# Kernel optimization log

Hardware: AMD Instinct MI355X
Metric: run time of the kernel (lower is better)

The kernel has to match this reference:

```python
import jax, jax.numpy as jnp
import numpy as np
from jax import lax

M, N, Q = 256, 65536, 64
LAMBDA_STAR = 0.1
LAMBDA_O = 0.1
T_ITERS = 16
PM_ITERS = 100


def setup_inputs() -> dict:
    key = jax.random.key(0)
    kx, kd = jax.random.split(key)
    X = jax.random.normal(kx, (M, N), dtype=jnp.float32)
    D = jax.random.normal(kd, (M, Q), dtype=jnp.float32)
    return {"X": X, "D": D}


def _power_method(D):
    # Largest eigenvalue of D^T D via 100-step power iteration (fixed random init).
    x0 = jax.random.normal(jax.random.key(1), (1, Q), dtype=D.dtype)

    def step(x, _):
        x = (x @ D.T) @ D          # [1,q] -> [1,m] -> [1,q]
        nm = jnp.linalg.norm(x)
        return x / nm, nm

    _, nms = lax.scan(step, x0, None, length=PM_ITERS)
    return nms[-1]


def reference(X, D):
    m, n = X.shape
    q = D.shape[1]
    alpha = _power_method(D)
    eta = 1.0 / alpha

    Iq = jnp.eye(q, dtype=D.dtype)
    Im = jnp.eye(m, dtype=D.dtype)
    top = jnp.concatenate([D.T @ D + LAMBDA_STAR * Iq, D.T], axis=1)   # [q, q+m]
    bot = jnp.concatenate([D, (1.0 + LAMBDA_STAR) * Im], axis=1)       # [m, q+m]
    H = jnp.eye(m + q, dtype=D.dtype) - eta * jnp.concatenate([top, bot], axis=0)
    W = eta * jnp.concatenate([D.T, Im], axis=0)                        # [(m+q), m]
    t = LAMBDA_O * eta * jnp.concatenate([jnp.zeros(q, D.dtype), jnp.ones(m, D.dtype)])

    b0 = W @ X                                                           # [(m+q), n]
    Z0 = jnp.zeros((m + q, n), dtype=X.dtype)

    def ista_step(carry, _):
        Z, b = carry
        Znew = jnp.maximum(0.0, b - t[:, None])    # thresholding (ger(t, ones) == t broadcast)
        b = b + H @ (Znew - Z)
        return (Znew, b), None

    (Z, _), _ = lax.scan(ista_step, (Z0, b0), None, length=T_ITERS)
    return Z
```

## Files before the change

kernel.cpp:

```cpp
#include <hip/hip_runtime.h>


typedef __bf16 bf16x8 __attribute__((ext_vector_type(8)));
typedef float f32x4 __attribute__((ext_vector_type(4)));

#define MFMA16(a, b, c) __builtin_amdgcn_mfma_f32_16x16x32_bf16((a), (b), (c), 0, 0, 0)

#define NTOT 65536
#define NCOL 32

__device__ __forceinline__ unsigned pk2(float a, float b) {
  unsigned short ua = __builtin_bit_cast(unsigned short, (__bf16)a);
  unsigned short ub = __builtin_bit_cast(unsigned short, (__bf16)b);
  return (unsigned)ua | ((unsigned)ub << 16);
}

__global__ void rnmf_prep(const float* __restrict__ D, void* __restrict__ ws) {
  float* wsf = (float*)ws;
  __bf16* Dbf = (__bf16*)((char*)ws + 256);
  __bf16* DTbf = (__bf16*)((char*)ws + 256 + 32768);

  __shared__ __bf16 DTl[64 * 264];
  __shared__ __bf16 gA[64 * 72];
  __shared__ __bf16 gB[64 * 72];
  __shared__ float gf[64 * 68];
  __shared__ __align__(16) float xv[64];

  const int tid = threadIdx.x;
  const int w = tid >> 6, lane = tid & 63, c = lane & 15, q4 = lane >> 4;

#pragma unroll
  for (int e = 0; e < 16; ++e) {
    int i4 = e * 256 + tid;
    float4 dv = *(const float4*)(D + i4 * 4);
    uint2 u; u.x = pk2(dv.x, dv.y); u.y = pk2(dv.z, dv.w);
    *(uint2*)(Dbf + i4 * 4) = u;
  }
#pragma unroll
  for (int e = 0; e < 64; ++e) {
    int flat = e * 256 + tid;
    int k = flat >> 6, a = flat & 63;
    DTl[a * 264 + k] = (__bf16)D[k * 64 + a];
  }
  __syncthreads();
#pragma unroll
  for (int e = 0; e < 8; ++e) {
    int fi = e * 256 + tid;
    int a = fi >> 5;
    int k = (fi * 8) & 255;
    *(bf16x8*)(DTbf + fi * 8) = *(const bf16x8*)&DTl[a * 264 + k];
  }
#pragma unroll
  for (int ct = 0; ct < 4; ++ct) {
    f32x4 acc = {0.f, 0.f, 0.f, 0.f};
#pragma unroll
    for (int kb = 0; kb < 8; ++kb) {
      bf16x8 a = *(const bf16x8*)&DTl[(16 * w + c) * 264 + 32 * kb + 8 * q4];
      bf16x8 b = *(const bf16x8*)&DTl[(16 * ct + c) * 264 + 32 * kb + 8 * q4];
      acc = MFMA16(a, b, acc);
    }
#pragma unroll
    for (int r = 0; r < 4; ++r)
      gA[(16 * w + 4 * q4 + r) * 72 + 16 * ct + c] = (__bf16)acc[r];
  }
  __syncthreads();
#pragma unroll
  for (int ct = 0; ct < 4; ++ct) {
    f32x4 acc = {0.f, 0.f, 0.f, 0.f};
#pragma unroll
    for (int kb = 0; kb < 2; ++kb) {
      bf16x8 a = *(const bf16x8*)&gA[(16 * w + c) * 72 + 32 * kb + 8 * q4];
      bf16x8 b = *(const bf16x8*)&gA[(16 * ct + c) * 72 + 32 * kb + 8 * q4];
      acc = MFMA16(a, b, acc);
    }
#pragma unroll
    for (int r = 0; r < 4; ++r)
      gB[(16 * w + 4 * q4 + r) * 72 + 16 * ct + c] = (__bf16)acc[r];
  }
  __syncthreads();
#pragma unroll
  for (int ct = 0; ct < 4; ++ct) {
    f32x4 acc = {0.f, 0.f, 0.f, 0.f};
#pragma unroll
    for (int kb = 0; kb < 2; ++kb) {
      bf16x8 a = *(const bf16x8*)&gB[(16 * w + c) * 72 + 32 * kb + 8 * q4];
      bf16x8 b = *(const bf16x8*)&gB[(16 * ct + c) * 72 + 32 * kb + 8 * q4];
      acc = MFMA16(a, b, acc);
    }
#pragma unroll
    for (int r = 0; r < 4; ++r)
      gA[(16 * w + 4 * q4 + r) * 72 + 16 * ct + c] = (__bf16)acc[r];
  }
  __syncthreads();
#pragma unroll
  for (int ct = 0; ct < 4; ++ct) {
    f32x4 acc = {0.f, 0.f, 0.f, 0.f};
#pragma unroll
    for (int kb = 0; kb < 2; ++kb) {
      bf16x8 a = *(const bf16x8*)&gA[(16 * w + c) * 72 + 32 * kb + 8 * q4];
      bf16x8 b = *(const bf16x8*)&gA[(16 * ct + c) * 72 + 32 * kb + 8 * q4];
      acc = MFMA16(a, b, acc);
    }
#pragma unroll
    for (int r = 0; r < 4; ++r)
      gf[(16 * w + 4 * q4 + r) * 68 + 16 * ct + c] = acc[r];
  }
  __syncthreads();

  if (w == 0) {
    float td = gf[lane * 68 + lane];
#pragma unroll
    for (int off = 32; off; off >>= 1) td += __shfl_xor(td, off, 64);
    const float tr = td;
    const float itr = 1.f / tr;
    xv[lane] = 1.f;
    float nm = 1.f;
    for (int itp = 0; itp < 28; ++itp) {
      float acc = 0.f;
#pragma unroll
      for (int k = 0; k < 64; k += 4) {
        float4 g = *(const float4*)&gf[lane * 68 + k];
        float4 xx = *(const float4*)&xv[k];
        acc = fmaf(g.x, xx.x, acc);
        acc = fmaf(g.y, xx.y, acc);
        acc = fmaf(g.z, xx.z, acc);
        acc = fmaf(g.w, xx.w, acc);
      }
      float y = acc * itr;
      float n2 = y * y;
#pragma unroll
      for (int off = 32; off; off >>= 1) n2 += __shfl_xor(n2, off, 64);
      nm = sqrtf(n2);
      xv[lane] = y / nm;
    }
    if (lane == 0) wsf[0] = 1.f / powf(nm * tr, 0.125f);
  }
}

__global__ __launch_bounds__(256, 2) void rnmf_main(const float* __restrict__ X,
                                                    float* __restrict__ Z,
                                                    const void* __restrict__ ws) {
  const float* wsf = (const float*)ws;
  const __bf16* Dbf = (const __bf16*)((const char*)ws + 256);
  const __bf16* DTbf = (const __bf16*)((const char*)ws + 256 + 32768);

  __shared__ __bf16 zqb[32 * 72];
  __shared__ __bf16 vb[32 * 264];
  __shared__ float xs[32 * 260];

  const int tid = threadIdx.x;
  const int w = tid >> 6;
  const int lane = tid & 63;
  const int c = lane & 15;
  const int q4 = lane >> 4;
  const int j0 = blockIdx.x * NCOL;

#pragma unroll
  for (int e = 0; e < 32; ++e) {
    int flat = e * 256 + tid;
    int row = flat >> 5, col = flat & 31;
    xs[col * 260 + row] = X[row * NTOT + j0 + col];
  }

  const float eta = wsf[0];
  const float cq = 1.f - 0.1f * eta;
  const float cm = 1.f - 1.1f * eta;
  const float tm = 0.1f * eta;

  bf16x8 d1[4][2];
#pragma unroll
  for (int rt = 0; rt < 4; ++rt)
#pragma unroll
    for (int kb = 0; kb < 2; ++kb)
      d1[rt][kb] = *(const bf16x8*)(Dbf + (64 * w + 16 * rt + c) * 64 + 32 * kb + 8 * q4);
  bf16x8 d2[8];
#pragma unroll
  for (int kb = 0; kb < 8; ++kb)
    d2[kb] = *(const bf16x8*)(DTbf + (16 * w + c) * 256 + 32 * kb + 8 * q4);

  __syncthreads();

  float bqt[2][4];
#pragma unroll
  for (int ct = 0; ct < 2; ++ct) {
    f32x4 acc = {0.f, 0.f, 0.f, 0.f};
#pragma unroll
    for (int kb = 0; kb < 8; ++kb) {
      const float* p = &xs[(16 * ct + c) * 260 + 32 * kb + 8 * q4];
      float4 lo = *(const float4*)p;
      float4 hi = *(const float4*)(p + 4);
      bf16x8 bf;
      bf[0] = (__bf16)lo.x; bf[1] = (__bf16)lo.y; bf[2] = (__bf16)lo.z; bf[3] = (__bf16)lo.w;
      bf[4] = (__bf16)hi.x; bf[5] = (__bf16)hi.y; bf[6] = (__bf16)hi.z; bf[7] = (__bf16)hi.w;
      acc = MFMA16(d2[kb], bf, acc);
    }
#pragma unroll
    for (int r = 0; r < 4; ++r) bqt[ct][r] = eta * acc[r];
  }

  float bmt[4][2][4];
#pragma unroll
  for (int rt = 0; rt < 4; ++rt)
#pragma unroll
    for (int ct = 0; ct < 2; ++ct) {
      const float* p = &xs[(16 * ct + c) * 260 + 64 * w + 16 * rt + 4 * q4];
      float4 v = *(const float4*)p;
      bmt[rt][ct][0] = fmaf(eta, v.x, -tm);
      bmt[rt][ct][1] = fmaf(eta, v.y, -tm);
      bmt[rt][ct][2] = fmaf(eta, v.z, -tm);
      bmt[rt][ct][3] = fmaf(eta, v.w, -tm);
    }

  float zq[2][4], zm[4][2][4];
#pragma unroll
  for (int ct = 0; ct < 2; ++ct)
#pragma unroll
    for (int r = 0; r < 4; ++r) zq[ct][r] = fmaxf(bqt[ct][r], 0.f);
#pragma unroll
  for (int rt = 0; rt < 4; ++rt)
#pragma unroll
    for (int ct = 0; ct < 2; ++ct)
#pragma unroll
      for (int r = 0; r < 4; ++r) zm[rt][ct][r] = fmaxf(bmt[rt][ct][r], 0.f);

#pragma unroll
  for (int ct = 0; ct < 2; ++ct) {
    uint2 u; u.x = pk2(zq[ct][0], zq[ct][1]); u.y = pk2(zq[ct][2], zq[ct][3]);
    *(uint2*)&zqb[(16 * ct + c) * 72 + 16 * w + 4 * q4] = u;
  }

  for (int it = 0; it < 15; ++it) {
    __syncthreads();
#pragma unroll
    for (int ct = 0; ct < 2; ++ct) {
      bf16x8 bz0 = *(const bf16x8*)&zqb[(16 * ct + c) * 72 + 8 * q4];
      bf16x8 bz1 = *(const bf16x8*)&zqb[(16 * ct + c) * 72 + 32 + 8 * q4];
#pragma unroll
      for (int rt = 0; rt < 4; ++rt) {
        f32x4 acc = {0.f, 0.f, 0.f, 0.f};
        acc = MFMA16(d1[rt][0], bz0, acc);
        acc = MFMA16(d1[rt][1], bz1, acc);
        float vv[4];
#pragma unroll
        for (int r = 0; r < 4; ++r) {
          float u = acc[r];
          float zo = zm[rt][ct][r];
          vv[r] = u + zo;
          float zn = fmaf(cm, zo, bmt[rt][ct][r]);
          zn = fmaf(-eta, u, zn);
          zm[rt][ct][r] = fmaxf(zn, 0.f);
        }
        uint2 uu; uu.x = pk2(vv[0], vv[1]); uu.y = pk2(vv[2], vv[3]);
        *(uint2*)&vb[(16 * ct + c) * 264 + 64 * w + 16 * rt + 4 * q4] = uu;
      }
    }
    __syncthreads();
#pragma unroll
    for (int ct = 0; ct < 2; ++ct) {
      f32x4 acc = {0.f, 0.f, 0.f, 0.f};
#pragma unroll
      for (int kb = 0; kb < 8; ++kb) {
        bf16x8 bv = *(const bf16x8*)&vb[(16 * ct + c) * 264 + 32 * kb + 8 * q4];
        acc = MFMA16(d2[kb], bv, acc);
      }
#pragma unroll
      for (int r = 0; r < 4; ++r) {
        float zn = fmaf(cq, zq[ct][r], bqt[ct][r]);
        zn = fmaf(-eta, acc[r], zn);
        zq[ct][r] = fmaxf(zn, 0.f);
      }
      uint2 u; u.x = pk2(zq[ct][0], zq[ct][1]); u.y = pk2(zq[ct][2], zq[ct][3]);
      *(uint2*)&zqb[(16 * ct + c) * 72 + 16 * w + 4 * q4] = u;
    }
  }

#pragma unroll
  for (int ct = 0; ct < 2; ++ct)
#pragma unroll
    for (int r = 0; r < 4; ++r)
      Z[(16 * w + 4 * q4 + r) * NTOT + j0 + 16 * ct + c] = zq[ct][r];
#pragma unroll
  for (int rt = 0; rt < 4; ++rt)
#pragma unroll
    for (int ct = 0; ct < 2; ++ct)
#pragma unroll
      for (int r = 0; r < 4; ++r)
        Z[(64 + 64 * w + 16 * rt + 4 * q4 + r) * NTOT + j0 + 16 * ct + c] = zm[rt][ct][r];
}

extern "C" void kernel_launch(void* const* d_in, const int* in_sizes, int n_in,
                              void* d_out, int out_size, void* d_ws, size_t ws_size,
                              hipStream_t stream) {
  const float* X = (const float*)d_in[0];
  const float* D = (const float*)d_in[1];
  float* Z = (float*)d_out;
  rnmf_prep<<<dim3(1), dim3(256), 0, stream>>>(D, d_ws);
  rnmf_main<<<dim3(NTOT / NCOL), dim3(256), 0, stream>>>(X, Z, d_ws);
}
```

Before: 243.4 us.

## Pack f32 math, reuse shared arena, fragment-order LDS layout, raise occupancy

The main kernel now puts all its shared buffers in one arena and reuses the X staging space for the z/v bf16 operands. Those operands are stored in MFMA fragment order, so each lane reads its 16 bytes contiguously. The elementwise ISTA update now uses packed two-wide f32 FMA/max with hardware bf16 pack conversion, X is loaded as float4, and launch bounds go from 2 to 3 blocks per CU. The prep kernel pads the Gram matrix rows to avoid LDS bank conflicts. Smaller LDS use and packed ALU ops aim at higher occupancy and fewer VALU instructions, at the cost of register pressure under the tighter bound.

```diff
diff --git a/kernel.cpp b/kernel.cpp
--- a/kernel.cpp
+++ b/kernel.cpp
@@ -2,7 +2,9 @@
 
 
 typedef __bf16 bf16x8 __attribute__((ext_vector_type(8)));
+typedef __bf16 bf16x2 __attribute__((ext_vector_type(2)));
 typedef float f32x4 __attribute__((ext_vector_type(4)));
+typedef float f32x2 __attribute__((ext_vector_type(2)));
 
 #define MFMA16(a, b, c) __builtin_amdgcn_mfma_f32_16x16x32_bf16((a), (b), (c), 0, 0, 0)
 
@@ -10,11 +12,24 @@
 #define NCOL 32
 
 __device__ __forceinline__ unsigned pk2(float a, float b) {
+#if __has_builtin(__builtin_amdgcn_cvt_pk_bf16_f32)
+  return __builtin_bit_cast(unsigned, __builtin_amdgcn_cvt_pk_bf16_f32(a, b));
+#else
   unsigned short ua = __builtin_bit_cast(unsigned short, (__bf16)a);
   unsigned short ub = __builtin_bit_cast(unsigned short, (__bf16)b);
   return (unsigned)ua | ((unsigned)ub << 16);
-}
-
+#endif
+}
+__device__ __forceinline__ unsigned pk2v(f32x2 v) { return pk2(v[0], v[1]); }
+__device__ __forceinline__ f32x2 f2(float s) { f32x2 v = {s, s}; return v; }
+__device__ __forceinline__ f32x2 pfma(f32x2 a, f32x2 b, f32x2 c) {
+  return __builtin_elementwise_fma(a, b, c);
+}
+__device__ __forceinline__ f32x2 pmax0(f32x2 a) {
+  return __builtin_elementwise_max(a, f2(0.f));
+}
+
+#define GOF(row) ((row) * 68 + (((row) >> 3) << 2))
 __global__ void rnmf_prep(const float* __restrict__ D, void* __restrict__ ws) {
   float* wsf = (float*)ws;
   __bf16* Dbf = (__bf16*)((char*)ws + 256);
@@ -23,7 +38,7 @@
   __shared__ __bf16 DTl[64 * 264];
   __shared__ __bf16 gA[64 * 72];
   __shared__ __bf16 gB[64 * 72];
-  __shared__ float gf[64 * 68];
+  __shared__ float gf[64 * 68 + 32];
   __shared__ __align__(16) float xv[64];
 
   const int tid = threadIdx.x;
@@ -103,23 +118,24 @@
     }
 #pragma unroll
     for (int r = 0; r < 4; ++r)
-      gf[(16 * w + 4 * q4 + r) * 68 + 16 * ct + c] = acc[r];
+      gf[GOF(16 * w + 4 * q4 + r) + 16 * ct + c] = acc[r];
   }
   __syncthreads();
 
   if (w == 0) {
-    float td = gf[lane * 68 + lane];
+    float td = gf[GOF(lane) + lane];
 #pragma unroll
     for (int off = 32; off; off >>= 1) td += __shfl_xor(td, off, 64);
     const float tr = td;
     const float itr = 1.f / tr;
     xv[lane] = 1.f;
     float nm = 1.f;
+    const int rowoff = GOF(lane);
     for (int itp = 0; itp < 28; ++itp) {
       float acc = 0.f;
 #pragma unroll
       for (int k = 0; k < 64; k += 4) {
-        float4 g = *(const float4*)&gf[lane * 68 + k];
+        float4 g = *(const float4*)&gf[rowoff + k];
         float4 xx = *(const float4*)&xv[k];
         acc = fmaf(g.x, xx.x, acc);
         acc = fmaf(g.y, xx.y, acc);
@@ -137,34 +153,40 @@
   }
 }
 
-__global__ __launch_bounds__(256, 2) void rnmf_main(const float* __restrict__ X,
+__global__ __launch_bounds__(256, 3) void rnmf_main(const float* __restrict__ X,
                                                     float* __restrict__ Z,
                                                     const void* __restrict__ ws) {
   const float* wsf = (const float*)ws;
   const __bf16* Dbf = (const __bf16*)((const char*)ws + 256);
   const __bf16* DTbf = (const __bf16*)((const char*)ws + 256 + 32768);
 
-  __shared__ __bf16 zqb[32 * 72];
-  __shared__ __bf16 vb[32 * 264];
-  __shared__ float xs[32 * 260];
+  __shared__ __align__(16) char arena[33280];
+  float* xs = (float*)arena;
 
   const int tid = threadIdx.x;
   const int w = tid >> 6;
   const int lane = tid & 63;
   const int c = lane & 15;
   const int q4 = lane >> 4;
+  const int q4h = q4 >> 1, q4l = q4 & 1;
   const int j0 = blockIdx.x * NCOL;
 
 #pragma unroll
-  for (int e = 0; e < 32; ++e) {
-    int flat = e * 256 + tid;
-    int row = flat >> 5, col = flat & 31;
-    xs[col * 260 + row] = X[row * NTOT + j0 + col];
+  for (int e = 0; e < 8; ++e) {
+    int idx = e * 256 + tid;
+    int row = idx >> 3, c4 = (idx & 7) * 4;
+    float4 g = *(const float4*)(X + row * NTOT + j0 + c4);
+    xs[(c4 + 0) * 260 + row] = g.x;
+    xs[(c4 + 1) * 260 + row] = g.y;
+    xs[(c4 + 2) * 260 + row] = g.z;
+    xs[(c4 + 3) * 260 + row] = g.w;
   }
 
   const float eta = wsf[0];
-  const float cq = 1.f - 0.1f * eta;
-  const float cm = 1.f - 1.1f * eta;
+  const f32x2 etav = f2(eta);
+  const f32x2 metav = f2(-eta);
+  const f32x2 cqv = f2(1.f - 0.1f * eta);
+  const f32x2 cmv = f2(1.f - 1.1f * eta);
   const float tm = 0.1f * eta;
 
   bf16x8 d1[4][2];
@@ -180,7 +202,7 @@
 
   __syncthreads();
 
-  float bqt[2][4];
+  f32x2 bqt2[2][2];
 #pragma unroll
   for (int ct = 0; ct < 2; ++ct) {
     f32x4 acc = {0.f, 0.f, 0.f, 0.f};
@@ -189,69 +211,73 @@
       const float* p = &xs[(16 * ct + c) * 260 + 32 * kb + 8 * q4];
       float4 lo = *(const float4*)p;
       float4 hi = *(const float4*)(p + 4);
-      bf16x8 bf;
-      bf[0] = (__bf16)lo.x; bf[1] = (__bf16)lo.y; bf[2] = (__bf16)lo.z; bf[3] = (__bf16)lo.w;
-      bf[4] = (__bf16)hi.x; bf[5] = (__bf16)hi.y; bf[6] = (__bf16)hi.z; bf[7] = (__bf16)hi.w;
-      acc = MFMA16(d2[kb], bf, acc);
-    }
-#pragma unroll
-    for (int r = 0; r < 4; ++r) bqt[ct][r] = eta * acc[r];
-  }
-
-  float bmt[4][2][4];
+      unsigned p0 = pk2(lo.x, lo.y), p1 = pk2(lo.z, lo.w);
+      unsigned p2 = pk2(hi.x, hi.y), p3 = pk2(hi.z, hi.w);
+      uint4 packed = {p0, p1, p2, p3};
+      acc = MFMA16(d2[kb], __builtin_bit_cast(bf16x8, packed), acc);
+    }
+    f32x2 a0 = {acc[0], acc[1]}, a1 = {acc[2], acc[3]};
+    bqt2[ct][0] = etav * a0;
+    bqt2[ct][1] = etav * a1;
+  }
+
+  f32x2 bmt2[4][2][2];
 #pragma unroll
   for (int rt = 0; rt < 4; ++rt)
 #pragma unroll
     for (int ct = 0; ct < 2; ++ct) {
       const float* p = &xs[(16 * ct + c) * 260 + 64 * w + 16 * rt + 4 * q4];
       float4 v = *(const float4*)p;
-      bmt[rt][ct][0] = fmaf(eta, v.x, -tm);
-      bmt[rt][ct][1] = fmaf(eta, v.y, -tm);
-      bmt[rt][ct][2] = fmaf(eta, v.z, -tm);
-      bmt[rt][ct][3] = fmaf(eta, v.w, -tm);
-    }
-
-  float zq[2][4], zm[4][2][4];
+      f32x2 x0 = {v.x, v.y}, x1 = {v.z, v.w};
+      bmt2[rt][ct][0] = pfma(etav, x0, f2(-tm));
+      bmt2[rt][ct][1] = pfma(etav, x1, f2(-tm));
+    }
+
+  __syncthreads();
+
+  f32x2 zq2[2][2], zm2[4][2][2];
 #pragma unroll
   for (int ct = 0; ct < 2; ++ct)
 #pragma unroll
-    for (int r = 0; r < 4; ++r) zq[ct][r] = fmaxf(bqt[ct][r], 0.f);
+    for (int p = 0; p < 2; ++p) zq2[ct][p] = pmax0(bqt2[ct][p]);
 #pragma unroll
   for (int rt = 0; rt < 4; ++rt)
 #pragma unroll
     for (int ct = 0; ct < 2; ++ct)
 #pragma unroll
-      for (int r = 0; r < 4; ++r) zm[rt][ct][r] = fmaxf(bmt[rt][ct][r], 0.f);
+      for (int p = 0; p < 2; ++p) zm2[rt][ct][p] = pmax0(bmt2[rt][ct][p]);
+
+  char* smem = arena;
+  const int rb = lane * 16;
+  const int wzq = (w >> 1) * 1024 + ((2 * w) & 3) * 256 + q4h * 256 + c * 16 + 8 * q4l;
+  const int wvb = 4096 + 2 * w * 1024 + q4h * 256 + c * 16 + 8 * q4l;
 
 #pragma unroll
   for (int ct = 0; ct < 2; ++ct) {
-    uint2 u; u.x = pk2(zq[ct][0], zq[ct][1]); u.y = pk2(zq[ct][2], zq[ct][3]);
-    *(uint2*)&zqb[(16 * ct + c) * 72 + 16 * w + 4 * q4] = u;
+    uint2 u; u.x = pk2v(zq2[ct][0]); u.y = pk2v(zq2[ct][1]);
+    *(uint2*)(smem + wzq + ct * 2048) = u;
   }
 
   for (int it = 0; it < 15; ++it) {
     __syncthreads();
 #pragma unroll
     for (int ct = 0; ct < 2; ++ct) {
-      bf16x8 bz0 = *(const bf16x8*)&zqb[(16 * ct + c) * 72 + 8 * q4];
-      bf16x8 bz1 = *(const bf16x8*)&zqb[(16 * ct + c) * 72 + 32 + 8 * q4];
+      bf16x8 bz0 = *(const bf16x8*)(smem + rb + ct * 2048);
+      bf16x8 bz1 = *(const bf16x8*)(smem + rb + ct * 2048 + 1024);
 #pragma unroll
       for (int rt = 0; rt < 4; ++rt) {
         f32x4 acc = {0.f, 0.f, 0.f, 0.f};
         acc = MFMA16(d1[rt][0], bz0, acc);
         acc = MFMA16(d1[rt][1], bz1, acc);
-        float vv[4];
-#pragma unroll
-        for (int r = 0; r < 4; ++r) {
-          float u = acc[r];
-          float zo = zm[rt][ct][r];
-          vv[r] = u + zo;
-          float zn = fmaf(cm, zo, bmt[rt][ct][r]);
-          zn = fmaf(-eta, u, zn);
-          zm[rt][ct][r] = fmaxf(zn, 0.f);
-        }
-        uint2 uu; uu.x = pk2(vv[0], vv[1]); uu.y = pk2(vv[2], vv[3]);
-        *(uint2*)&vb[(16 * ct + c) * 264 + 64 * w + 16 * rt + 4 * q4] = uu;
+        f32x2 u0 = {acc[0], acc[1]}, u1 = {acc[2], acc[3]};
+        f32x2 z0 = zm2[rt][ct][0], z1 = zm2[rt][ct][1];
+        f32x2 v0 = u0 + z0, v1 = u1 + z1;
+        f32x2 t0 = pfma(cmv, z0, bmt2[rt][ct][0]);
+        f32x2 t1 = pfma(cmv, z1, bmt2[rt][ct][1]);
+        zm2[rt][ct][0] = pmax0(pfma(metav, u0, t0));
+        zm2[rt][ct][1] = pmax0(pfma(metav, u1, t1));
+        uint2 uu; uu.x = pk2v(v0); uu.y = pk2v(v1);
+        *(uint2*)(smem + wvb + ct * 8192 + rt * 512) = uu;
       }
     }
     __syncthreads();
@@ -260,32 +286,35 @@
       f32x4 acc = {0.f, 0.f, 0.f, 0.f};
 #pragma unroll
       for (int kb = 0; kb < 8; ++kb) {
-        bf16x8 bv = *(const bf16x8*)&vb[(16 * ct + c) * 264 + 32 * kb + 8 * q4];
+        bf16x8 bv = *(const bf16x8*)(smem + rb + 4096 + ct * 8192 + kb * 1024);
         acc = MFMA16(d2[kb], bv, acc);
       }
-#pragma unroll
-      for (int r = 0; r < 4; ++r) {
-        float zn = fmaf(cq, zq[ct][r], bqt[ct][r]);
-        zn = fmaf(-eta, acc[r], zn);
-        zq[ct][r] = fmaxf(zn, 0.f);
-      }
-      uint2 u; u.x = pk2(zq[ct][0], zq[ct][1]); u.y = pk2(zq[ct][2], zq[ct][3]);
-      *(uint2*)&zqb[(16 * ct + c) * 72 + 16 * w + 4 * q4] = u;
+      f32x2 w0 = {acc[0], acc[1]}, w1 = {acc[2], acc[3]};
+      f32x2 t0 = pfma(cqv, zq2[ct][0], bqt2[ct][0]);
+      f32x2 t1 = pfma(cqv, zq2[ct][1], bqt2[ct][1]);
+      zq2[ct][0] = pmax0(pfma(metav, w0, t0));
+      zq2[ct][1] = pmax0(pfma(metav, w1, t1));
+      uint2 u; u.x = pk2v(zq2[ct][0]); u.y = pk2v(zq2[ct][1]);
+      *(uint2*)(smem + wzq + ct * 2048) = u;
     }
   }
 
 #pragma unroll
   for (int ct = 0; ct < 2; ++ct)
 #pragma unroll
-    for (int r = 0; r < 4; ++r)
-      Z[(16 * w + 4 * q4 + r) * NTOT + j0 + 16 * ct + c] = zq[ct][r];
+    for (int p = 0; p < 2; ++p)
+#pragma unroll
+      for (int e = 0; e < 2; ++e)
+        Z[(16 * w + 4 * q4 + 2 * p + e) * NTOT + j0 + 16 * ct + c] = zq2[ct][p][e];
 #pragma unroll
   for (int rt = 0; rt < 4; ++rt)
 #pragma unroll
     for (int ct = 0; ct < 2; ++ct)
 #pragma unroll
-      for (int r = 0; r < 4; ++r)
-        Z[(64 + 64 * w + 16 * rt + 4 * q4 + r) * NTOT + j0 + 16 * ct + c] = zm[rt][ct][r];
+      for (int p = 0; p < 2; ++p)
+#pragma unroll
+        for (int e = 0; e < 2; ++e)
+          Z[(64 + 64 * w + 16 * rt + 4 * q4 + 2 * p + e) * NTOT + j0 + 16 * ct + c] = zm2[rt][ct][p][e];
 }
 
 extern "C" void kernel_launch(void* const* d_in, const int* in_sizes, int n_in,
```

Result: faster. 229.6 us (-5.7%).
